# Optimization experiments

Measured on AMD Instinct MI355X. Metric: run time of the kernel, lower is better.

## Reference

```python
import jax, jax.numpy as jnp
import numpy as np

DEPTH = 4  # truncation depth of the signature


def setup_inputs() -> dict:
    key = jax.random.key(0)
    # path: (batch, stream, channels)
    path = jax.random.normal(key, (128, 128, 12), dtype=jnp.float32)
    return {"path": path}


def _exp_terms(d, depth):
    """Tensor exponential of a single linear increment d: (B, C).

    Returns a tuple of flattened levels; level k has shape (B, C**k) and
    equals d^{\otimes k} / k!.
    """
    B = d.shape[0]
    terms = [d]
    for k in range(2, depth + 1):
        terms.append(jnp.einsum('bi,bj->bij', terms[-1], d).reshape(B, -1) / k)
    return tuple(terms)


def _signature(path, depth):
    """Truncated path signature (stream=False, basepoint=False).

    Combines per-increment tensor exponentials with Chen's identity:
    (A \otimes B)_m = A_m + B_m + sum_{i=1}^{m-1} A_i \otimes B_{m-i}.
    """
    B, L, C = path.shape
    dx = path[:, 1:] - path[:, :-1]  # (B, L-1, C) path increments
    init = _exp_terms(dx[:, 0], depth)

    def step(sig, d):
        e = _exp_terms(d, depth)
        new = []
        for m in range(1, depth + 1):  # signature level m, shape (B, C**m)
            t = sig[m - 1] + e[m - 1]
            for i in range(1, m):  # cross terms sig_i (x) e_{m-i}
                t = t + jnp.einsum('bi,bj->bij', sig[i - 1], e[m - i - 1]).reshape(B, -1)
            new.append(t)
        return tuple(new), None

    # scan over the remaining L-2 increments (time-major)
    sig, _ = jax.lax.scan(step, init, jnp.transpose(dx[:, 1:], (1, 0, 2)))
    # flatten levels in order 1..depth, matching signatory's layout
    return jnp.concatenate(sig, axis=-1)  # (B, C + C^2 + ... + C^depth)


def reference(path):
    return _signature(path, DEPTH)
```

## Files before the change

### kernel.cpp

```cpp
#include <hip/hip_runtime.h>


#define NC    12
#define NPTS  128
#define OUT_PER_B 22620
#define BLOCK 448
#define PADQ  33

__device__ __forceinline__ float rl(float v, int lane) {
    return __int_as_float(__builtin_amdgcn_readlane(__float_as_int(v), lane));
}

__global__ __launch_bounds__(BLOCK, 4)
void sig_kernel(const float* __restrict__ path, float* __restrict__ out) {
    const int bid = blockIdx.x;
    const int b  = bid >> 2;
    const int q  = bid & 3;
    const int jq = q >> 1;
    const int kq = q & 1;
    const int t  = threadIdx.x;

    __shared__ __align__(16) float4 DT4[NC * PADQ];
    __shared__ __align__(16) float4 P4[NPTS * NC / 4];

    const float4* pb4 = (const float4*)(path + (size_t)b * (NPTS * NC));
    if (t < 384) P4[t] = pb4[t];
    __syncthreads();
    if (t < 384) {
        const int c  = t >> 5;
        const int sq = t & 31;
        const float* P = (const float*)P4;
        float d[4];
        #pragma unroll
        for (int e = 0; e < 4; ++e) {
            int s = 4 * sq + e;
            d[e] = (s < NPTS - 1) ? (P[(s + 1) * NC + c] - P[s * NC + c]) : 0.f;
        }
        DT4[c * PADQ + sq] = make_float4(d[0], d[1], d[2], d[3]);
    }
    __syncthreads();

    const int ta  = (t < 432) ? t : (t - 432);
    const int i   = ta / 36;
    const int r   = ta - i * 36;
    const int jl  = r / 6;
    const int kl  = r - jl * 6;
    const int j   = jq * 6 + jl;
    const int k   = kq * 6 + kl;

    float acc[12];
    #pragma unroll
    for (int l = 0; l < 12; ++l) acc[l] = 0.f;
    float s3 = 0.f, s2 = 0.f, s1 = 0.f;

    const int lane = t & 63;
    const float4* dti = &DT4[i * PADQ];
    const float4* dtj = &DT4[j * PADQ];
    const float4* dtk = &DT4[k * PADQ];
    const float4* dtv = &DT4[(lane < 12 ? lane : 11) * PADQ];

    for (int sq = 0; sq < 32; ++sq) {
        float4 di4 = dti[sq];
        float4 dj4 = dtj[sq];
        float4 dk4 = dtk[sq];
        float4 dv4 = dtv[sq];

        #pragma unroll
        for (int u = 0; u < 4; ++u) {
            const float di = (&di4.x)[u];
            const float dj = (&dj4.x)[u];
            const float dk = (&dk4.x)[u];
            const float dv = (&dv4.x)[u];

            float A4 = (s1 + 0.25f * di) * (1.f / 3.f);
            float B4 = (s2 + dj * A4) * 0.5f;
            float C3 = s3 + dk * B4;

            #pragma unroll
            for (int l = 0; l < 12; ++l)
                acc[l] += C3 * rl(dv, l);

            float A3 = (s1 + di * (1.f / 3.f)) * 0.5f;
            float C2 = s2 + dj * A3;
            s3 += dk * C2;
            s2 += dj * (s1 + 0.5f * di);
            s1 += di;
        }
    }

    if (t < 432) {
        float* ob = out + (size_t)b * OUT_PER_B;
        if (q == 0 && jl == 0 && kl == 0) ob[i] = s1;
        if (kl == 0) ob[12 + i * 12 + j] = s2;
        const int ijk = (i * 12 + j) * 12 + k;
        ob[156 + ijk] = s3;
        float4* o4 = (float4*)(ob + 1884 + (size_t)ijk * 12);
        o4[0] = make_float4(acc[0], acc[1], acc[2],  acc[3]);
        o4[1] = make_float4(acc[4], acc[5], acc[6],  acc[7]);
        o4[2] = make_float4(acc[8], acc[9], acc[10], acc[11]);
    }
}

extern "C" void kernel_launch(void* const* d_in, const int* in_sizes, int n_in,
                              void* d_out, int out_size, void* d_ws, size_t ws_size,
                              hipStream_t stream) {
    const float* path = (const float*)d_in[0];
    float* out = (float*)d_out;
    const int nbatch = in_sizes[0] / (NPTS * NC);
    sig_kernel<<<nbatch * 4, BLOCK, 0, stream>>>(path, out);
}
```

Baseline: 89.81 us.

## Register-tile four k indices per thread and read l-increments from row-major LDS

Each thread now computes four k values times twelve l outputs for a fixed (i,j), so the level-1/2 prefix terms are shared across the four k values. The per-lane readlane broadcasts are replaced by float4 reads from a new row-major copy of the increments in shared memory. Blocks shrink to 128 threads with 108 active, which cuts redundant scalar recurrence work. The cost is much lower wave-level parallelism and a longer serial chain per thread.

```diff
diff --git a/kernel.cpp b/kernel.cpp
--- a/kernel.cpp
+++ b/kernel.cpp
@@ -4,100 +4,119 @@
 #define NC    12
 #define NPTS  128
 #define OUT_PER_B 22620
-#define BLOCK 448
+#define BLOCK 128
 #define PADQ  33
 
-__device__ __forceinline__ float rl(float v, int lane) {
-    return __int_as_float(__builtin_amdgcn_readlane(__float_as_int(v), lane));
-}
-
-__global__ __launch_bounds__(BLOCK, 4)
+__global__ __launch_bounds__(BLOCK, 2)
 void sig_kernel(const float* __restrict__ path, float* __restrict__ out) {
     const int bid = blockIdx.x;
     const int b  = bid >> 2;
-    const int q  = bid & 3;
-    const int jq = q >> 1;
-    const int kq = q & 1;
+    const int iq = bid & 3;
     const int t  = threadIdx.x;
 
+    __shared__ __align__(16) float4 P4[384];
     __shared__ __align__(16) float4 DT4[NC * PADQ];
-    __shared__ __align__(16) float4 P4[NPTS * NC / 4];
+    __shared__ __align__(16) float  Drow[NPTS * NC];
 
     const float4* pb4 = (const float4*)(path + (size_t)b * (NPTS * NC));
-    if (t < 384) P4[t] = pb4[t];
+    #pragma unroll
+    for (int v = 0; v < 3; ++v) P4[t + 128 * v] = pb4[t + 128 * v];
     __syncthreads();
-    if (t < 384) {
-        const int c  = t >> 5;
-        const int sq = t & 31;
+    {
         const float* P = (const float*)P4;
-        float d[4];
         #pragma unroll
-        for (int e = 0; e < 4; ++e) {
-            int s = 4 * sq + e;
-            d[e] = (s < NPTS - 1) ? (P[(s + 1) * NC + c] - P[s * NC + c]) : 0.f;
+        for (int v = 0; v < 3; ++v) {
+            int idx = t + 128 * v;
+            int c  = idx >> 5;
+            int sq = idx & 31;
+            float d[4];
+            #pragma unroll
+            for (int e = 0; e < 4; ++e) {
+                int s = 4 * sq + e;
+                d[e] = (s < NPTS - 1) ? (P[(s + 1) * NC + c] - P[s * NC + c]) : 0.f;
+                Drow[s * NC + c] = d[e];
+            }
+            DT4[c * PADQ + sq] = make_float4(d[0], d[1], d[2], d[3]);
         }
-        DT4[c * PADQ + sq] = make_float4(d[0], d[1], d[2], d[3]);
     }
     __syncthreads();
 
-    const int ta  = (t < 432) ? t : (t - 432);
-    const int i   = ta / 36;
-    const int r   = ta - i * 36;
-    const int jl  = r / 6;
-    const int kl  = r - jl * 6;
-    const int j   = jq * 6 + jl;
-    const int k   = kq * 6 + kl;
+    if (t < 108) {
+        const int il = t / 36;
+        const int r  = t - il * 36;
+        const int j  = r / 3;
+        const int kq = r - j * 3;
+        const int i  = iq * 3 + il;
+        const int k0 = kq * 4;
 
-    float acc[12];
-    #pragma unroll
-    for (int l = 0; l < 12; ++l) acc[l] = 0.f;
-    float s3 = 0.f, s2 = 0.f, s1 = 0.f;
+        float acc[4][12];
+        #pragma unroll
+        for (int q = 0; q < 4; ++q)
+            #pragma unroll
+            for (int l = 0; l < 12; ++l) acc[q][l] = 0.f;
+        float s3[4] = {0.f, 0.f, 0.f, 0.f};
+        float s2 = 0.f, s1 = 0.f;
 
-    const int lane = t & 63;
-    const float4* dti = &DT4[i * PADQ];
-    const float4* dtj = &DT4[j * PADQ];
-    const float4* dtk = &DT4[k * PADQ];
-    const float4* dtv = &DT4[(lane < 12 ? lane : 11) * PADQ];
+        const float4* dti  = &DT4[i * PADQ];
+        const float4* dtj  = &DT4[j * PADQ];
+        const float4* dtk0 = &DT4[(k0 + 0) * PADQ];
+        const float4* dtk1 = &DT4[(k0 + 1) * PADQ];
+        const float4* dtk2 = &DT4[(k0 + 2) * PADQ];
+        const float4* dtk3 = &DT4[(k0 + 3) * PADQ];
 
-    for (int sq = 0; sq < 32; ++sq) {
-        float4 di4 = dti[sq];
-        float4 dj4 = dtj[sq];
-        float4 dk4 = dtk[sq];
-        float4 dv4 = dtv[sq];
-
-        #pragma unroll
-        for (int u = 0; u < 4; ++u) {
-            const float di = (&di4.x)[u];
-            const float dj = (&dj4.x)[u];
-            const float dk = (&dk4.x)[u];
-            const float dv = (&dv4.x)[u];
-
-            float A4 = (s1 + 0.25f * di) * (1.f / 3.f);
-            float B4 = (s2 + dj * A4) * 0.5f;
-            float C3 = s3 + dk * B4;
+        for (int sq = 0; sq < 32; ++sq) {
+            float4 di4 = dti[sq];
+            float4 dj4 = dtj[sq];
+            float4 dka = dtk0[sq];
+            float4 dkb = dtk1[sq];
+            float4 dkc = dtk2[sq];
+            float4 dkd = dtk3[sq];
+            const float4* dvp = (const float4*)&Drow[sq * 48];
 
             #pragma unroll
-            for (int l = 0; l < 12; ++l)
-                acc[l] += C3 * rl(dv, l);
+            for (int u = 0; u < 4; ++u) {
+                float4 va = dvp[3 * u + 0];
+                float4 vb = dvp[3 * u + 1];
+                float4 vc = dvp[3 * u + 2];
 
-            float A3 = (s1 + di * (1.f / 3.f)) * 0.5f;
-            float C2 = s2 + dj * A3;
-            s3 += dk * C2;
-            s2 += dj * (s1 + 0.5f * di);
-            s1 += di;
+                const float di = (&di4.x)[u];
+                const float dj = (&dj4.x)[u];
+
+                float A4 = (s1 + 0.25f * di) * (1.f / 3.f);
+                float B4 = (s2 + dj * A4) * 0.5f;
+                float A3 = (s1 + di * (1.f / 3.f)) * 0.5f;
+                float C2 = s2 + dj * A3;
+
+                float dk[4] = {(&dka.x)[u], (&dkb.x)[u], (&dkc.x)[u], (&dkd.x)[u]};
+                #pragma unroll
+                for (int q = 0; q < 4; ++q) {
+                    float C3 = s3[q] + dk[q] * B4;
+                    acc[q][0]  += C3 * va.x;  acc[q][1]  += C3 * va.y;
+                    acc[q][2]  += C3 * va.z;  acc[q][3]  += C3 * va.w;
+                    acc[q][4]  += C3 * vb.x;  acc[q][5]  += C3 * vb.y;
+                    acc[q][6]  += C3 * vb.z;  acc[q][7]  += C3 * vb.w;
+                    acc[q][8]  += C3 * vc.x;  acc[q][9]  += C3 * vc.y;
+                    acc[q][10] += C3 * vc.z;  acc[q][11] += C3 * vc.w;
+                    s3[q] += dk[q] * C2;
+                }
+                s2 += dj * (s1 + 0.5f * di);
+                s1 += di;
+            }
         }
-    }
 
-    if (t < 432) {
         float* ob = out + (size_t)b * OUT_PER_B;
-        if (q == 0 && jl == 0 && kl == 0) ob[i] = s1;
-        if (kl == 0) ob[12 + i * 12 + j] = s2;
-        const int ijk = (i * 12 + j) * 12 + k;
-        ob[156 + ijk] = s3;
+        if (j == 0 && kq == 0) ob[i] = s1;
+        if (kq == 0) ob[12 + i * 12 + j] = s2;
+        const int ijk = (i * 12 + j) * 12 + k0;
+        #pragma unroll
+        for (int q = 0; q < 4; ++q) ob[156 + ijk + q] = s3[q];
         float4* o4 = (float4*)(ob + 1884 + (size_t)ijk * 12);
-        o4[0] = make_float4(acc[0], acc[1], acc[2],  acc[3]);
-        o4[1] = make_float4(acc[4], acc[5], acc[6],  acc[7]);
-        o4[2] = make_float4(acc[8], acc[9], acc[10], acc[11]);
+        #pragma unroll
+        for (int q = 0; q < 4; ++q) {
+            o4[3 * q + 0] = make_float4(acc[q][0], acc[q][1], acc[q][2],  acc[q][3]);
+            o4[3 * q + 1] = make_float4(acc[q][4], acc[q][5], acc[q][6],  acc[q][7]);
+            o4[3 * q + 2] = make_float4(acc[q][8], acc[q][9], acc[q][10], acc[q][11]);
+        }
     }
 }
 
```

Result: faster. 82.94 us (-7.6%).
